# Optimization experiments

Measured on AMD Instinct MI355X. Metric: run time of the kernel, lower is better.

Reference implementation:

```python
import jax, jax.numpy as jnp
import numpy as np

# fixed-point config (matches init_kwargs)
DIM, H = 768, 12
DHEAD = DIM // H
DATA_W, DATA_F = 32, 16        # input activation quantizer
WQ = WK = WV = WP = (16, 8)    # weight quantizers (width, frac)
BQ = BK = BV = BP = (16, 8)    # bias quantizers
DQ = DK = DV = DS = DZ = (16, 8)  # activation quantizers after each stage
OUT_W, OUT_F = 32, 8


def qfix(x, width, frac):
    """Fixed-point integer quantizer: round to 2^-frac grid, clamp to signed width."""
    scale = jnp.float32(2.0 ** frac)
    lo = -(2.0 ** (width - 1))
    hi = 2.0 ** (width - 1) - 1
    return jnp.clip(jnp.round(x * scale), lo, hi) / scale


def setup_inputs() -> dict:
    key = jax.random.key(0)
    ks = jax.random.split(key, 5)
    return {
        "q_in": jax.random.normal(ks[0], (2, 2048, DIM), dtype=jnp.float32),
        "wqkv": jax.random.normal(ks[1], (3 * DIM, DIM), dtype=jnp.float32) * 0.05,
        "bqkv": jax.random.normal(ks[2], (3 * DIM,), dtype=jnp.float32) * 0.05,
        "wp": jax.random.normal(ks[3], (DIM, DIM), dtype=jnp.float32) * 0.05,
        "bp": jax.random.normal(ks[4], (DIM,), dtype=jnp.float32) * 0.05,
    }


def reference(q_in, wqkv, bqkv, wp, bp):
    B, N, _ = q_in.shape
    # per-head weight split: wqkv -> (H, 3*DHEAD, DIM), rows [0:d]=q, [d:2d]=k, [2d:3d]=v
    w = wqkv.reshape(H, 3 * DHEAD, DIM)
    b = bqkv.reshape(H, 3 * DHEAD)
    wq_, wk_, wv_ = w[:, :DHEAD], w[:, DHEAD:2 * DHEAD], w[:, 2 * DHEAD:]
    bq_, bk_, bv_ = b[:, :DHEAD], b[:, DHEAD:2 * DHEAD], b[:, 2 * DHEAD:]

    x = qfix(q_in, DATA_W, DATA_F)  # QuantizedLinear input quantization

    def qlin(wt, bt, wcfg, bcfg, ocfg):
        # y[b,h,n,e] = x[b,n,d] @ qw[h,e,d]^T + qb[h,e], then output quantize
        y = jnp.einsum('bnd,hed->bhne', x, qfix(wt, *wcfg)) + qfix(bt, *bcfg)[None, :, None, :]
        return qfix(y, *ocfg)

    q = qlin(wq_, bq_, WQ, BQ, DQ)  # (B,H,N,DHEAD)
    k = qlin(wk_, bk_, WK, BK, DK)
    v = qlin(wv_, bv_, WV, BV, DV)

    s = qfix(jnp.einsum('bhne,bhme->bhnm', q, k), *DS)   # (B,H,N,N) quantized scores
    z = qfix(jnp.einsum('bhnm,bhme->bhne', s, v), *DZ)   # (B,H,N,DHEAD)

    # concat heads along feature dim (torch.cat dim=2)
    zc = z.transpose(0, 2, 1, 3).reshape(B, N, DIM)

    # quantized projection: input quantized with data_z cfg (idempotent here)
    out = jnp.einsum('bnd,ed->bne', qfix(zc, *DZ), qfix(wp, *WP)) + qfix(bp, *BP)
    return qfix(out, OUT_W, OUT_F)
```

## Files before the change

kernel.cpp:

```cpp
#include <hip/hip_runtime.h>


#define NTOK 4096
#define DIM  768
#define NH   12
#define DH   64
#define SEQ  2048
#define QKVD 2304
#define NBH  24
#define LSTR 72
#define KVBUF (64 * LSTR * 2 * 2)

typedef _Float16 half8 __attribute__((ext_vector_type(8)));
typedef _Float16 half4 __attribute__((ext_vector_type(4)));
typedef __fp16   fp16x2 __attribute__((ext_vector_type(2)));
typedef float floatx4 __attribute__((ext_vector_type(4)));
typedef float floatx16 __attribute__((ext_vector_type(16)));

#define GLOAD16(gsrc, ldst) \
    __builtin_amdgcn_global_load_lds( \
        (const __attribute__((address_space(1))) void*)(gsrc), \
        (__attribute__((address_space(3))) void*)(ldst), 16, 0, 0)

__global__ __launch_bounds__(256) void prep(
    const float* __restrict__ X,
    const float* __restrict__ wqkv, const float* __restrict__ bqkv,
    const float* __restrict__ wp,   const float* __restrict__ bp,
    _Float16* __restrict__ Xh, _Float16* __restrict__ Xl,
    _Float16* __restrict__ W16, _Float16* __restrict__ Wp16,
    float* __restrict__ bq24, float* __restrict__ bp16)
{
    int i = blockIdx.x * 256 + threadIdx.x;
    int i4 = i * 4;
    if (i4 < NTOK * DIM) {
        float4 x = *(const float4*)(X + i4);
        float xi[4] = {x.x, x.y, x.z, x.w};
        half4 oh, ol;
#pragma unroll
        for (int j = 0; j < 4; ++j) {
            float v = rintf(xi[j] * 65536.0f);
            float h = rintf(v * (1.0f / 2048.0f));
            ((_Float16*)&oh)[j] = (_Float16)h;
            ((_Float16*)&ol)[j] = (_Float16)(v - 2048.0f * h);
        }
        *(half4*)(Xh + i4) = oh;
        *(half4*)(Xl + i4) = ol;
    }
    if (i4 < QKVD * DIM) {
        float4 w = *(const float4*)(wqkv + i4);
        half4 o = {(_Float16)rintf(w.x * 256.0f), (_Float16)rintf(w.y * 256.0f),
                   (_Float16)rintf(w.z * 256.0f), (_Float16)rintf(w.w * 256.0f)};
        *(half4*)(W16 + i4) = o;
    }
    if (i4 < DIM * DIM) {
        float4 w = *(const float4*)(wp + i4);
        half4 o = {(_Float16)rintf(w.x * 256.0f), (_Float16)rintf(w.y * 256.0f),
                   (_Float16)rintf(w.z * 256.0f), (_Float16)rintf(w.w * 256.0f)};
        *(half4*)(Wp16 + i4) = o;
    }
    if (i < QKVD) bq24[i] = rintf(bqkv[i] * 256.0f) * 65536.0f;
    if (i < DIM)  bp16[i] = rintf(bp[i] * 256.0f) * 256.0f;
}

__global__ __launch_bounds__(256, 4) void qkv_mfma(
    const _Float16* __restrict__ Xh, const _Float16* __restrict__ Xl,
    const _Float16* __restrict__ W16, const float* __restrict__ bq24,
    _Float16* __restrict__ Q16, _Float16* __restrict__ K16,
    _Float16* __restrict__ Vt16)
{
    __shared__ __align__(16) _Float16 Ah[64 * 64];
    __shared__ __align__(16) _Float16 Al[64 * 64];
    __shared__ __align__(16) _Float16 Bs[128 * 64];
    const int t = threadIdx.x;
    const int w = t >> 6, lane = t & 63;
    const int l31 = lane & 31, hi = lane >> 5;
    const int wr = w >> 1;
    const int wc = w & 1;
    const int m0 = blockIdx.x * 64;
    const int col0 = blockIdx.y * 128;

    const int lr = lane >> 3;
    const int lg8 = ((lane & 7) ^ lr) * 8;

    floatx16 acch[2], accl[2];
#pragma unroll
    for (int ct = 0; ct < 2; ++ct)
#pragma unroll
        for (int r = 0; r < 16; ++r) { acch[ct][r] = 0.f; accl[ct][r] = 0.f; }

    for (int k0 = 0; k0 < DIM; k0 += 64) {
        __syncthreads();
        GLOAD16(Xh + (size_t)(m0 + 16 * w + lr) * DIM + k0 + lg8,
                &Ah[(2 * w) * 512]);
        GLOAD16(Xh + (size_t)(m0 + 16 * w + 8 + lr) * DIM + k0 + lg8,
                &Ah[(2 * w + 1) * 512]);
        GLOAD16(Xl + (size_t)(m0 + 16 * w + lr) * DIM + k0 + lg8,
                &Al[(2 * w) * 512]);
        GLOAD16(Xl + (size_t)(m0 + 16 * w + 8 + lr) * DIM + k0 + lg8,
                &Al[(2 * w + 1) * 512]);
#pragma unroll
        for (int q = 0; q < 4; ++q) {
            GLOAD16(W16 + (size_t)(col0 + 32 * w + 8 * q + lr) * DIM + k0 + lg8,
                    &Bs[(4 * w + q) * 512]);
        }
        __syncthreads();
#pragma unroll
        for (int i = 0; i < 4; ++i) {
            const int arow = 32 * wr + l31;
            const int g = 2 * i + hi;
            half8 ah = *(const half8*)(&Ah[arow * 64 + ((g ^ (arow & 7)) << 3)]);
            half8 al = *(const half8*)(&Al[arow * 64 + ((g ^ (arow & 7)) << 3)]);
#pragma unroll
            for (int ct = 0; ct < 2; ++ct) {
                const int brow = 64 * wc + 32 * ct + l31;
                half8 bf = *(const half8*)(&Bs[brow * 64 + ((g ^ (brow & 7)) << 3)]);
                acch[ct] = __builtin_amdgcn_mfma_f32_32x32x16_f16(ah, bf, acch[ct], 0, 0, 0);
                accl[ct] = __builtin_amdgcn_mfma_f32_32x32x16_f16(al, bf, accl[ct], 0, 0, 0);
            }
        }
    }

    const int b_ = m0 >> 11;
    const int nbase = (m0 & 2047) + 32 * wr;
#pragma unroll
    for (int ct = 0; ct < 2; ++ct) {
        const int c = col0 + 64 * wc + 32 * ct + l31;
        const int h = c / 192;
        const int jj = c % 192;
        const int kind = jj >> 6;
        const int e = jj & 63;
        const int bh = b_ * NH + h;
        const float bb = bq24[c];
        float qv[16];
#pragma unroll
        for (int r = 0; r < 16; ++r) {
            float y = fmaf(2048.0f, acch[ct][r], accl[ct][r]) + bb;
            float q = rintf(y * (1.0f / 65536.0f));
            qv[r] = fminf(fmaxf(q, -32768.0f), 32767.0f);
        }
        if (kind == 2) {
#pragma unroll
            for (int g = 0; g < 4; ++g) {
                int nv = nbase + 16 * (g >> 1) + 8 * hi + 4 * (g & 1);
                half4 o = {(_Float16)qv[4 * g + 0], (_Float16)qv[4 * g + 1],
                           (_Float16)qv[4 * g + 2], (_Float16)qv[4 * g + 3]};
                *(half4*)(Vt16 + ((size_t)bh * DH + e) * SEQ + nv) = o;
            }
        } else {
            _Float16* dst = (kind == 0) ? Q16 : K16;
#pragma unroll
            for (int r = 0; r < 16; ++r) {
                int er = (r & 3) + 8 * (r >> 2) + 4 * hi;
                dst[((size_t)bh * SEQ + nbase + er) * DH + e] = (_Float16)qv[r];
            }
        }
    }
}

__global__ __launch_bounds__(256, 3) void attention_mfma(
    const _Float16* __restrict__ Q16, const _Float16* __restrict__ K16,
    const _Float16* __restrict__ Vt16,
    _Float16* __restrict__ Zh16, _Float16* __restrict__ Zl16)
{
    __shared__ __align__(16) char smem[2 * KVBUF];
    float* scr = (float*)smem;

    const int t = threadIdx.x;
    const int bh = blockIdx.x;
    const int qt = blockIdx.y;
    const int w = t >> 6, lane = t & 63;
    const int l31 = lane & 31, hi = lane >> 5;
    const int wj = w & 1;
    const int wi = w >> 1;
    const int sr = t >> 3, sk8 = t & 7;
    const _Float16* Qg = Q16 + ((size_t)bh * SEQ + qt * 64) * DH;
    const _Float16* Kg = K16 + (size_t)bh * SEQ * DH;
    const _Float16* Vg = Vt16 + (size_t)bh * DH * SEQ;

    half8 qf[4];
#pragma unroll
    for (int i = 0; i < 4; ++i)
        qf[i] = *(const half8*)(Qg + (32 * wj + l31) * DH + 16 * i + 8 * hi);

    half8 pk0, pk1, pv0, pv1;
    pk0 = *(const half8*)(Kg + (size_t)sr * DH + sk8 * 8);
    pk1 = *(const half8*)(Kg + (size_t)(sr + 32) * DH + sk8 * 8);
    pv0 = *(const half8*)(Vg + (size_t)sr * SEQ + sk8 * 8);
    pv1 = *(const half8*)(Vg + (size_t)(sr + 32) * SEQ + sk8 * 8);
    {
        _Float16* Ks = (_Float16*)smem;
        _Float16* Vs = Ks + 64 * LSTR;
        *(half8*)(&Ks[sr * LSTR + sk8 * 8]) = pk0;
        *(half8*)(&Ks[(sr + 32) * LSTR + sk8 * 8]) = pk1;
        *(half8*)(&Vs[sr * LSTR + sk8 * 8]) = pv0;
        *(half8*)(&Vs[(sr + 32) * LSTR + sk8 * 8]) = pv1;
    }

    floatx16 acc0h, acc0l, acc1h, acc1l;
#pragma unroll
    for (int r = 0; r < 16; ++r) { acc0h[r] = 0.f; acc0l[r] = 0.f; acc1h[r] = 0.f; acc1l[r] = 0.f; }

    for (int it = 0; it < 32; ++it) {
        _Float16* Ks = (_Float16*)(smem + (it & 1) * KVBUF);
        _Float16* Vs = Ks + 64 * LSTR;
        __syncthreads();

        if (it < 31) {
            const int mn = (it + 1) * 64;
            pk0 = *(const half8*)(Kg + (size_t)(mn + sr) * DH + sk8 * 8);
            pk1 = *(const half8*)(Kg + (size_t)(mn + sr + 32) * DH + sk8 * 8);
            pv0 = *(const half8*)(Vg + (size_t)sr * SEQ + mn + sk8 * 8);
            pv1 = *(const half8*)(Vg + (size_t)(sr + 32) * SEQ + mn + sk8 * 8);
        }

        floatx16 sc;
#pragma unroll
        for (int r = 0; r < 16; ++r) sc[r] = 0.f;
        __builtin_amdgcn_s_setprio(1);
#pragma unroll
        for (int i = 0; i < 4; ++i) {
            half8 kf = *(const half8*)(&Ks[(32 * wi + l31) * LSTR + 16 * i + 8 * hi]);
            sc = __builtin_amdgcn_mfma_f32_32x32x16_f16(kf, qf[i], sc, 0, 0, 0);
        }
        __builtin_amdgcn_s_setprio(0);

        float hh[16], ll[16];
#pragma unroll
        for (int r = 0; r < 16; ++r) {
            float v = rintf(sc[r] * 0.00390625f);
            v = fminf(fmaxf(v, -32768.0f), 32767.0f);
            float h = rintf(v * (1.0f / 2048.0f));
            hh[r] = h;
            ll[r] = fmaf(-2048.0f, h, v);
        }
        int dwh[4][2], dwl[4][2];
        union { fp16x2 h; int i; } cv;
#pragma unroll
        for (int g = 0; g < 4; ++g) {
            cv.h = __builtin_amdgcn_cvt_pkrtz(hh[4 * g + 0], hh[4 * g + 1]); dwh[g][0] = cv.i;
            cv.h = __builtin_amdgcn_cvt_pkrtz(hh[4 * g + 2], hh[4 * g + 3]); dwh[g][1] = cv.i;
            cv.h = __builtin_amdgcn_cvt_pkrtz(ll[4 * g + 0], ll[4 * g + 1]); dwl[g][0] = cv.i;
            cv.h = __builtin_amdgcn_cvt_pkrtz(ll[4 * g + 2], ll[4 * g + 3]); dwl[g][1] = cv.i;
        }

        half8 vf[2][2];
#pragma unroll
        for (int et = 0; et < 2; ++et)
#pragma unroll
            for (int c = 0; c < 2; ++c)
                vf[et][c] = *(const half8*)(&Vs[(32 * et + l31) * LSTR + 32 * wi + 16 * c + 8 * hi]);
        __builtin_amdgcn_s_setprio(1);
#pragma unroll
        for (int c = 0; c < 2; ++c) {
            union { int b[4]; half8 v; } ubh, ubl;
            ubh.b[0] = dwh[2 * c][0];     ubh.b[1] = dwh[2 * c][1];
            ubh.b[2] = dwh[2 * c + 1][0]; ubh.b[3] = dwh[2 * c + 1][1];
            ubl.b[0] = dwl[2 * c][0];     ubl.b[1] = dwl[2 * c][1];
            ubl.b[2] = dwl[2 * c + 1][0]; ubl.b[3] = dwl[2 * c + 1][1];
            acc0h = __builtin_amdgcn_mfma_f32_32x32x16_f16(vf[0][c], ubh.v, acc0h, 0, 0, 0);
            acc0l = __builtin_amdgcn_mfma_f32_32x32x16_f16(vf[0][c], ubl.v, acc0l, 0, 0, 0);
            acc1h = __builtin_amdgcn_mfma_f32_32x32x16_f16(vf[1][c], ubh.v, acc1h, 0, 0, 0);
            acc1l = __builtin_amdgcn_mfma_f32_32x32x16_f16(vf[1][c], ubl.v, acc1l, 0, 0, 0);
        }
        __builtin_amdgcn_s_setprio(0);

        if (it < 31) {
            _Float16* Kn = (_Float16*)(smem + ((it + 1) & 1) * KVBUF);
            _Float16* Vn = Kn + 64 * LSTR;
            *(half8*)(&Kn[sr * LSTR + sk8 * 8]) = pk0;
            *(half8*)(&Kn[(sr + 32) * LSTR + sk8 * 8]) = pk1;
            *(half8*)(&Vn[sr * LSTR + sk8 * 8]) = pv0;
            *(half8*)(&Vn[(sr + 32) * LSTR + sk8 * 8]) = pv1;
        }
    }

    float zfh[16], zfl[16];
    {
        __syncthreads();
#pragma unroll
        for (int r = 0; r < 16; ++r) {
            int er = (r & 3) + 8 * (r >> 2) + 4 * hi;
            float sendh = wi ? acc0h[r] : acc1h[r];
            scr[((wj * 2 + (1 - wi)) * 32 + er) * 33 + l31] = sendh;
        }
        __syncthreads();
#pragma unroll
        for (int r = 0; r < 16; ++r) {
            int er = (r & 3) + 8 * (r >> 2) + 4 * hi;
            float keeph = wi ? acc1h[r] : acc0h[r];
            zfh[r] = keeph + scr[((wj * 2 + wi) * 32 + er) * 33 + l31];
        }
        __syncthreads();
#pragma unroll
        for (int r = 0; r < 16; ++r) {
            int er = (r & 3) + 8 * (r >> 2) + 4 * hi;
            float sendl = wi ? acc0l[r] : acc1l[r];
            scr[((wj * 2 + (1 - wi)) * 32 + er) * 33 + l31] = sendl;
        }
        __syncthreads();
#pragma unroll
        for (int r = 0; r < 16; ++r) {
            int er = (r & 3) + 8 * (r >> 2) + 4 * hi;
            float keepl = wi ? acc1l[r] : acc0l[r];
            zfl[r] = keepl + scr[((wj * 2 + wi) * 32 + er) * 33 + l31];
        }
    }

    const int b_ = bh / NH, h = bh % NH;
    const int n = qt * 64 + 32 * wj + l31;
    const size_t rowoff = ((size_t)b_ * SEQ + n) * DIM + h * DH;
#pragma unroll
    for (int g = 0; g < 4; ++g) {
        int e0 = 32 * wi + 8 * g + 4 * hi;
        half4 ph, pl;
#pragma unroll
        for (int j = 0; j < 4; ++j) {
            int r = 4 * g + j;
            float zint = fmaf(2048.0f, zfh[r], zfl[r]);
            float zq = rintf(zint * 0.00390625f);
            zq = fminf(fmaxf(zq, -32768.0f), 32767.0f);
            float zdh = rintf(zq * (1.0f / 2048.0f));
            ((_Float16*)&ph)[j] = (_Float16)zdh;
            ((_Float16*)&pl)[j] = (_Float16)(zq - 2048.0f * zdh);
        }
        *(half4*)(Zh16 + rowoff + e0) = ph;
        *(half4*)(Zl16 + rowoff + e0) = pl;
    }
}

__global__ __launch_bounds__(256) void out_mfma(
    const _Float16* __restrict__ Zh, const _Float16* __restrict__ Zl,
    const _Float16* __restrict__ Wp16, const float* __restrict__ bp16,
    float* __restrict__ O)
{
    __shared__ __align__(16) _Float16 Ah[64 * 64];
    __shared__ __align__(16) _Float16 Al[64 * 64];
    __shared__ __align__(16) _Float16 Bs[128 * 64];
    const int t = threadIdx.x;
    const int wave = t >> 6, lane = t & 63;
    const int lrow = lane & 15, quad = lane >> 4;
    const int m0 = blockIdx.y * 64;
    const int col0 = blockIdx.x * 128;

    const int lr = lane >> 3;
    const int lg8 = ((lane & 7) ^ lr) * 8;

    floatx4 acch[4][2], accl[4][2];
#pragma unroll
    for (int fm = 0; fm < 4; ++fm)
#pragma unroll
        for (int fn = 0; fn < 2; ++fn) {
            acch[fm][fn] = (floatx4){0.f, 0.f, 0.f, 0.f};
            accl[fm][fn] = (floatx4){0.f, 0.f, 0.f, 0.f};
        }

    for (int k0 = 0; k0 < DIM; k0 += 64) {
        __syncthreads();
        GLOAD16(Zh + (size_t)(m0 + 16 * wave + lr) * DIM + k0 + lg8,
                &Ah[(2 * wave) * 512]);
        GLOAD16(Zh + (size_t)(m0 + 16 * wave + 8 + lr) * DIM + k0 + lg8,
                &Ah[(2 * wave + 1) * 512]);
        GLOAD16(Zl + (size_t)(m0 + 16 * wave + lr) * DIM + k0 + lg8,
                &Al[(2 * wave) * 512]);
        GLOAD16(Zl + (size_t)(m0 + 16 * wave + 8 + lr) * DIM + k0 + lg8,
                &Al[(2 * wave + 1) * 512]);
#pragma unroll
        for (int q = 0; q < 4; ++q) {
            GLOAD16(Wp16 + (size_t)(col0 + 32 * wave + 8 * q + lr) * DIM + k0 + lg8,
                    &Bs[(4 * wave + q) * 512]);
        }
        __syncthreads();
#pragma unroll
        for (int kk = 0; kk < 64; kk += 32) {
            const int g = (kk >> 3) + quad;
            half8 bf[2];
#pragma unroll
            for (int fn = 0; fn < 2; ++fn) {
                const int br = wave * 32 + fn * 16 + lrow;
                bf[fn] = *(const half8*)(&Bs[br * 64 + ((g ^ (br & 7)) << 3)]);
            }
#pragma unroll
            for (int fm = 0; fm < 4; ++fm) {
                const int ar = fm * 16 + lrow;
                half8 ah = *(const half8*)(&Ah[ar * 64 + ((g ^ (ar & 7)) << 3)]);
                half8 al = *(const half8*)(&Al[ar * 64 + ((g ^ (ar & 7)) << 3)]);
#pragma unroll
                for (int fn = 0; fn < 2; ++fn) {
                    acch[fm][fn] = __builtin_amdgcn_mfma_f32_16x16x32_f16(ah, bf[fn], acch[fm][fn], 0, 0, 0);
                    accl[fm][fn] = __builtin_amdgcn_mfma_f32_16x16x32_f16(al, bf[fn], accl[fm][fn], 0, 0, 0);
                }
            }
        }
    }

#pragma unroll
    for (int fn = 0; fn < 2; ++fn) {
        const int c = col0 + wave * 32 + fn * 16 + lrow;
        const float bb = bp16[c];
#pragma unroll
        for (int fm = 0; fm < 4; ++fm)
#pragma unroll
            for (int rg = 0; rg < 4; ++rg) {
                float y = fmaf(2048.0f, acch[fm][fn][rg], accl[fm][fn][rg]) + bb;
                float o = rintf(y * 0.00390625f) * 0.00390625f;
                int r = m0 + fm * 16 + quad * 4 + rg;
                O[(size_t)r * DIM + c] = o;
            }
    }
}

extern "C" void kernel_launch(void* const* d_in, const int* in_sizes, int n_in,
                              void* d_out, int out_size, void* d_ws, size_t ws_size,
                              hipStream_t stream) {
    const float* q_in = (const float*)d_in[0];
    const float* wqkv = (const float*)d_in[1];
    const float* bqkv = (const float*)d_in[2];
    const float* wp   = (const float*)d_in[3];
    const float* bp   = (const float*)d_in[4];

    char* w = (char*)d_ws;
    _Float16* W16  = (_Float16*)w;  w += (size_t)QKVD * DIM * 2;
    _Float16* Wp16 = (_Float16*)w;  w += (size_t)DIM * DIM * 2;
    float* bq24    = (float*)w;     w += QKVD * 4;
    float* bp16    = (float*)w;     w += DIM * 4;
    _Float16* Xh   = (_Float16*)w;  w += (size_t)NTOK * DIM * 2;
    _Float16* Xl   = (_Float16*)w;  w += (size_t)NTOK * DIM * 2;
    _Float16* Q16  = (_Float16*)w;  w += (size_t)NBH * SEQ * DH * 2;
    _Float16* K16  = (_Float16*)w;  w += (size_t)NBH * SEQ * DH * 2;
    _Float16* Vt16 = (_Float16*)w;  w += (size_t)NBH * SEQ * DH * 2;
    _Float16* Zh16 = (_Float16*)w;  w += (size_t)NTOK * DIM * 2;
    _Float16* Zl16 = (_Float16*)w;  w += (size_t)NTOK * DIM * 2;
    (void)ws_size; (void)in_sizes; (void)n_in; (void)out_size;

    prep<<<dim3(NTOK * DIM / 4 / 256), 256, 0, stream>>>(
        q_in, wqkv, bqkv, wp, bp, Xh, Xl, W16, Wp16, bq24, bp16);
    qkv_mfma<<<dim3(NTOK / 64, QKVD / 128), 256, 0, stream>>>(
        Xh, Xl, W16, bq24, Q16, K16, Vt16);
    attention_mfma<<<dim3(NBH, SEQ / 64), 256, 0, stream>>>(Q16, K16, Vt16, Zh16, Zl16);
    out_mfma<<<dim3(DIM / 128, NTOK / 64), 256, 0, stream>>>(
        Zh16, Zl16, Wp16, bp16, (float*)d_out);
}
```

Baseline: 180.0 us.

## Load K/V fragments directly from global memory, dropping LDS staging and barriers

The attention kernel no longer stages K and V tiles through double-buffered shared memory with a per-iteration __syncthreads. Each wave now loads its MFMA operand fragments straight from global memory, relying on L2/cache reuse across waves and blocks. This removes the LDS writes, LDS reads and block barriers in the main loop. In exchange, global traffic goes up because two waves share the same K rows, and the software prefetch is lost, so load latency is now exposed unless the compiler or occupancy hides it.

```diff
diff --git a/kernel.cpp b/kernel.cpp
--- a/kernel.cpp
+++ b/kernel.cpp
@@ -8,8 +8,6 @@
 #define SEQ  2048
 #define QKVD 2304
 #define NBH  24
-#define LSTR 72
-#define KVBUF (64 * LSTR * 2 * 2)
 
 typedef _Float16 half8 __attribute__((ext_vector_type(8)));
 typedef _Float16 half4 __attribute__((ext_vector_type(4)));
@@ -162,8 +160,7 @@
     const _Float16* __restrict__ Vt16,
     _Float16* __restrict__ Zh16, _Float16* __restrict__ Zl16)
 {
-    __shared__ __align__(16) char smem[2 * KVBUF];
-    float* scr = (float*)smem;
+    __shared__ __align__(16) float scr[4 * 32 * 33];
 
     const int t = threadIdx.x;
     const int bh = blockIdx.x;
@@ -172,7 +169,6 @@
     const int l31 = lane & 31, hi = lane >> 5;
     const int wj = w & 1;
     const int wi = w >> 1;
-    const int sr = t >> 3, sk8 = t & 7;
     const _Float16* Qg = Q16 + ((size_t)bh * SEQ + qt * 64) * DH;
     const _Float16* Kg = K16 + (size_t)bh * SEQ * DH;
     const _Float16* Vg = Vt16 + (size_t)bh * DH * SEQ;
@@ -182,35 +178,23 @@
     for (int i = 0; i < 4; ++i)
         qf[i] = *(const half8*)(Qg + (32 * wj + l31) * DH + 16 * i + 8 * hi);
 
-    half8 pk0, pk1, pv0, pv1;
-    pk0 = *(const half8*)(Kg + (size_t)sr * DH + sk8 * 8);
-    pk1 = *(const half8*)(Kg + (size_t)(sr + 32) * DH + sk8 * 8);
-    pv0 = *(const half8*)(Vg + (size_t)sr * SEQ + sk8 * 8);
-    pv1 = *(const half8*)(Vg + (size_t)(sr + 32) * SEQ + sk8 * 8);
-    {
-        _Float16* Ks = (_Float16*)smem;
-        _Float16* Vs = Ks + 64 * LSTR;
-        *(half8*)(&Ks[sr * LSTR + sk8 * 8]) = pk0;
-        *(half8*)(&Ks[(sr + 32) * LSTR + sk8 * 8]) = pk1;
-        *(half8*)(&Vs[sr * LSTR + sk8 * 8]) = pv0;
-        *(half8*)(&Vs[(sr + 32) * LSTR + sk8 * 8]) = pv1;
-    }
+    const _Float16* Kw  = Kg + (size_t)(32 * wi + l31) * DH + 8 * hi;
+    const _Float16* Vw0 = Vg + (size_t)(l31) * SEQ + 32 * wi + 8 * hi;
+    const _Float16* Vw1 = Vg + (size_t)(32 + l31) * SEQ + 32 * wi + 8 * hi;
 
     floatx16 acc0h, acc0l, acc1h, acc1l;
 #pragma unroll
     for (int r = 0; r < 16; ++r) { acc0h[r] = 0.f; acc0l[r] = 0.f; acc1h[r] = 0.f; acc1l[r] = 0.f; }
 
-    for (int it = 0; it < 32; ++it) {
-        _Float16* Ks = (_Float16*)(smem + (it & 1) * KVBUF);
-        _Float16* Vs = Ks + 64 * LSTR;
-        __syncthreads();
-
-        if (it < 31) {
-            const int mn = (it + 1) * 64;
-            pk0 = *(const half8*)(Kg + (size_t)(mn + sr) * DH + sk8 * 8);
-            pk1 = *(const half8*)(Kg + (size_t)(mn + sr + 32) * DH + sk8 * 8);
-            pv0 = *(const half8*)(Vg + (size_t)sr * SEQ + mn + sk8 * 8);
-            pv1 = *(const half8*)(Vg + (size_t)(sr + 32) * SEQ + mn + sk8 * 8);
+    for (int m0 = 0; m0 < SEQ; m0 += 64) {
+        half8 kf[4], vf0[2], vf1[2];
+#pragma unroll
+        for (int i = 0; i < 4; ++i)
+            kf[i] = *(const half8*)(Kw + (size_t)m0 * DH + 16 * i);
+#pragma unroll
+        for (int c = 0; c < 2; ++c) {
+            vf0[c] = *(const half8*)(Vw0 + m0 + 16 * c);
+            vf1[c] = *(const half8*)(Vw1 + m0 + 16 * c);
         }
 
         floatx16 sc;
@@ -218,10 +202,8 @@
         for (int r = 0; r < 16; ++r) sc[r] = 0.f;
         __builtin_amdgcn_s_setprio(1);
 #pragma unroll
-        for (int i = 0; i < 4; ++i) {
-            half8 kf = *(const half8*)(&Ks[(32 * wi + l31) * LSTR + 16 * i + 8 * hi]);
-            sc = __builtin_amdgcn_mfma_f32_32x32x16_f16(kf, qf[i], sc, 0, 0, 0);
-        }
+        for (int i = 0; i < 4; ++i)
+            sc = __builtin_amdgcn_mfma_f32_32x32x16_f16(kf[i], qf[i], sc, 0, 0, 0);
         __builtin_amdgcn_s_setprio(0);
 
         float hh[16], ll[16];
@@ -243,12 +225,6 @@
             cv.h = __builtin_amdgcn_cvt_pkrtz(ll[4 * g + 2], ll[4 * g + 3]); dwl[g][1] = cv.i;
         }
 
-        half8 vf[2][2];
-#pragma unroll
-        for (int et = 0; et < 2; ++et)
-#pragma unroll
-            for (int c = 0; c < 2; ++c)
-                vf[et][c] = *(const half8*)(&Vs[(32 * et + l31) * LSTR + 32 * wi + 16 * c + 8 * hi]);
         __builtin_amdgcn_s_setprio(1);
 #pragma unroll
         for (int c = 0; c < 2; ++c) {
@@ -257,21 +233,12 @@
             ubh.b[2] = dwh[2 * c + 1][0]; ubh.b[3] = dwh[2 * c + 1][1];
             ubl.b[0] = dwl[2 * c][0];     ubl.b[1] = dwl[2 * c][1];
             ubl.b[2] = dwl[2 * c + 1][0]; ubl.b[3] = dwl[2 * c + 1][1];
-            acc0h = __builtin_amdgcn_mfma_f32_32x32x16_f16(vf[0][c], ubh.v, acc0h, 0, 0, 0);
-            acc0l = __builtin_amdgcn_mfma_f32_32x32x16_f16(vf[0][c], ubl.v, acc0l, 0, 0, 0);
-            acc1h = __builtin_amdgcn_mfma_f32_32x32x16_f16(vf[1][c], ubh.v, acc1h, 0, 0, 0);
-            acc1l = __builtin_amdgcn_mfma_f32_32x32x16_f16(vf[1][c], ubl.v, acc1l, 0, 0, 0);
+            acc0h = __builtin_amdgcn_mfma_f32_32x32x16_f16(vf0[c], ubh.v, acc0h, 0, 0, 0);
+            acc0l = __builtin_amdgcn_mfma_f32_32x32x16_f16(vf0[c], ubl.v, acc0l, 0, 0, 0);
+            acc1h = __builtin_amdgcn_mfma_f32_32x32x16_f16(vf1[c], ubh.v, acc1h, 0, 0, 0);
+            acc1l = __builtin_amdgcn_mfma_f32_32x32x16_f16(vf1[c], ubl.v, acc1l, 0, 0, 0);
         }
         __builtin_amdgcn_s_setprio(0);
-
-        if (it < 31) {
-            _Float16* Kn = (_Float16*)(smem + ((it + 1) & 1) * KVBUF);
-            _Float16* Vn = Kn + 64 * LSTR;
-            *(half8*)(&Kn[sr * LSTR + sk8 * 8]) = pk0;
-            *(half8*)(&Kn[(sr + 32) * LSTR + sk8 * 8]) = pk1;
-            *(half8*)(&Vn[sr * LSTR + sk8 * 8]) = pv0;
-            *(half8*)(&Vn[(sr + 32) * LSTR + sk8 * 8]) = pv1;
-        }
     }
 
     float zfh[16], zfl[16];
```

Measured after the change: 223.6 us. 24.3% more time.

## Double-buffer QKV GEMM LDS tiles with prefetch of next K chunk

Applied to the files above, without the earlier changes.

Splits the QKV projection's K loop into 32-wide chunks held in two LDS buffers. The loads for the next chunk are issued before the MFMAs on the current one, which replaces two barriers per 64-wide step with one barrier per 32-wide step. The XOR swizzle is changed to suit the 32-column rows. This aims to hide global-to-LDS latency behind compute, at the cost of more iterations and barriers in total and a new bank-conflict pattern.

```diff
diff --git a/kernel.cpp b/kernel.cpp
--- a/kernel.cpp
+++ b/kernel.cpp
@@ -68,9 +68,9 @@
     _Float16* __restrict__ Q16, _Float16* __restrict__ K16,
     _Float16* __restrict__ Vt16)
 {
-    __shared__ __align__(16) _Float16 Ah[64 * 64];
-    __shared__ __align__(16) _Float16 Al[64 * 64];
-    __shared__ __align__(16) _Float16 Bs[128 * 64];
+    __shared__ __align__(16) _Float16 Ah[2][64 * 32];
+    __shared__ __align__(16) _Float16 Al[2][64 * 32];
+    __shared__ __align__(16) _Float16 Bs[2][128 * 32];
     const int t = threadIdx.x;
     const int w = t >> 6, lane = t & 63;
     const int l31 = lane & 31, hi = lane >> 5;
@@ -79,8 +79,19 @@
     const int m0 = blockIdx.x * 64;
     const int col0 = blockIdx.y * 128;
 
-    const int lr = lane >> 3;
-    const int lg8 = ((lane & 7) ^ lr) * 8;
+    const int srow = lane >> 2;
+    const int sg8 = (((lane & 3) ^ ((lane >> 3) & 3)) << 3);
+
+#define QSTAGE(bi, kc) do { \
+    GLOAD16(Xh + (size_t)(m0 + 16 * w + srow) * DIM + (kc) + sg8, \
+            &Ah[bi][(16 * w) * 32]); \
+    GLOAD16(Xl + (size_t)(m0 + 16 * w + srow) * DIM + (kc) + sg8, \
+            &Al[bi][(16 * w) * 32]); \
+    GLOAD16(W16 + (size_t)(col0 + 32 * w + srow) * DIM + (kc) + sg8, \
+            &Bs[bi][(32 * w) * 32]); \
+    GLOAD16(W16 + (size_t)(col0 + 32 * w + 16 + srow) * DIM + (kc) + sg8, \
+            &Bs[bi][(32 * w + 16) * 32]); \
+} while (0)
 
     floatx16 acch[2], accl[2];
 #pragma unroll
@@ -88,37 +99,30 @@
 #pragma unroll
         for (int r = 0; r < 16; ++r) { acch[ct][r] = 0.f; accl[ct][r] = 0.f; }
 
-    for (int k0 = 0; k0 < DIM; k0 += 64) {
-        __syncthreads();
-        GLOAD16(Xh + (size_t)(m0 + 16 * w + lr) * DIM + k0 + lg8,
-                &Ah[(2 * w) * 512]);
-        GLOAD16(Xh + (size_t)(m0 + 16 * w + 8 + lr) * DIM + k0 + lg8,
-                &Ah[(2 * w + 1) * 512]);
-        GLOAD16(Xl + (size_t)(m0 + 16 * w + lr) * DIM + k0 + lg8,
-                &Al[(2 * w) * 512]);
-        GLOAD16(Xl + (size_t)(m0 + 16 * w + 8 + lr) * DIM + k0 + lg8,
-                &Al[(2 * w + 1) * 512]);
-#pragma unroll
-        for (int q = 0; q < 4; ++q) {
-            GLOAD16(W16 + (size_t)(col0 + 32 * w + 8 * q + lr) * DIM + k0 + lg8,
-                    &Bs[(4 * w + q) * 512]);
-        }
-        __syncthreads();
-#pragma unroll
-        for (int i = 0; i < 4; ++i) {
+    QSTAGE(0, 0);
+    __syncthreads();
+
+    for (int kt = 0; kt < 24; ++kt) {
+        const int bi = kt & 1;
+        if (kt < 23) QSTAGE(bi ^ 1, (kt + 1) * 32);
+
+#pragma unroll
+        for (int i = 0; i < 2; ++i) {
             const int arow = 32 * wr + l31;
             const int g = 2 * i + hi;
-            half8 ah = *(const half8*)(&Ah[arow * 64 + ((g ^ (arow & 7)) << 3)]);
-            half8 al = *(const half8*)(&Al[arow * 64 + ((g ^ (arow & 7)) << 3)]);
+            half8 ah = *(const half8*)(&Ah[bi][arow * 32 + ((g ^ ((arow >> 1) & 3)) << 3)]);
+            half8 al = *(const half8*)(&Al[bi][arow * 32 + ((g ^ ((arow >> 1) & 3)) << 3)]);
 #pragma unroll
             for (int ct = 0; ct < 2; ++ct) {
                 const int brow = 64 * wc + 32 * ct + l31;
-                half8 bf = *(const half8*)(&Bs[brow * 64 + ((g ^ (brow & 7)) << 3)]);
+                half8 bf = *(const half8*)(&Bs[bi][brow * 32 + ((g ^ ((brow >> 1) & 3)) << 3)]);
                 acch[ct] = __builtin_amdgcn_mfma_f32_32x32x16_f16(ah, bf, acch[ct], 0, 0, 0);
                 accl[ct] = __builtin_amdgcn_mfma_f32_32x32x16_f16(al, bf, accl[ct], 0, 0, 0);
             }
         }
-    }
+        __syncthreads();
+    }
+#undef QSTAGE
 
     const int b_ = m0 >> 11;
     const int nbase = (m0 & 2047) + 32 * wr;
```

Result: slower. 185.8 us (+3.2%).
